# Performance work log

Measured on AMD Instinct MI355X. Metric: run time of the kernel, lower is better.

Reference implementation:

```python
import jax, jax.numpy as jnp
import numpy as np

EMBED = 1024
HEADS = 16
HDIM = 64
FFN = 4 * EMBED
EPS = 1e-5


def setup_inputs() -> dict:
    key = jax.random.key(0)
    ks = jax.random.split(key, 12)
    def lin(k, fan_in, shape):
        b = 1.0 / np.sqrt(fan_in)
        return jax.random.uniform(k, shape, jnp.float32, -b, b)
    return {
        "x": jax.random.normal(ks[0], (4, 2048, EMBED), jnp.float32),
        "Wq": lin(ks[1], EMBED, (EMBED, HEADS * HDIM)),
        "Wk": lin(ks[2], EMBED, (EMBED, HEADS * HDIM)),
        "Wv": lin(ks[3], EMBED, (EMBED, HEADS * HDIM)),
        "Wo": lin(ks[4], HEADS * HDIM, (HEADS * HDIM, EMBED)),
        "ln1_g": jnp.ones((EMBED,), jnp.float32),
        "ln1_b": jnp.zeros((EMBED,), jnp.float32),
        "ln2_g": jnp.ones((EMBED,), jnp.float32),
        "ln2_b": jnp.zeros((EMBED,), jnp.float32),
        "W1": lin(ks[5], EMBED, (EMBED, FFN)),
        "b1": lin(ks[6], EMBED, (FFN,)),
        "W2": lin(ks[7], FFN, (FFN, EMBED)),
        "b2": lin(ks[8], FFN, (EMBED,)),
    }


def _layer_norm(x, g, b):
    mu = jnp.mean(x, axis=-1, keepdims=True)
    var = jnp.var(x, axis=-1, keepdims=True)
    return (x - mu) * jax.lax.rsqrt(var + EPS) * g + b


def reference(x, Wq, Wk, Wv, Wo, ln1_g, ln1_b, ln2_g, ln2_b, W1, b1, W2, b2):
    B, S, _ = x.shape
    residual = x
    h = _layer_norm(x, ln1_g, ln1_b)
    # project and split heads: [B, H, S, Dh]
    q = (h @ Wq).reshape(B, S, HEADS, HDIM).transpose(0, 2, 1, 3)
    k = (h @ Wk).reshape(B, S, HEADS, HDIM).transpose(0, 2, 1, 3)
    v = (h @ Wv).reshape(B, S, HEADS, HDIM).transpose(0, 2, 1, 3)
    scale = HDIM ** -0.5
    scores = jnp.einsum("bhqd,bhkd->bhqk", q, k) * scale
    # causal mask (upper triangle excluded above diagonal -> -inf)
    mask = jnp.triu(jnp.ones((S, S), bool), k=1)
    scores = jnp.where(mask, -jnp.inf, scores)
    attn = jax.nn.softmax(scores, axis=-1)
    out = jnp.einsum("bhqk,bhkd->bhqd", attn, v)
    out = out.transpose(0, 2, 1, 3).reshape(B, S, HEADS * HDIM)
    x = residual + out @ Wo
    residual = x
    h = _layer_norm(x, ln2_g, ln2_b)
    h = jax.nn.gelu(h @ W1 + b1, approximate=False) @ W2 + b2
    return residual + h
```

## Files before the change

kernel.cpp:

```cpp
#include <hip/hip_runtime.h>
#include <hip/hip_bf16.h>
#include <math.h>

typedef __bf16 bf16;
typedef bf16 bf16x8 __attribute__((ext_vector_type(8)));
typedef bf16 bf16x4 __attribute__((ext_vector_type(4)));
typedef float f32x4 __attribute__((ext_vector_type(4)));

#define ROWS 8192
#define EMB  1024
#define NH   16
#define HD   64
#define FFN  4096
#define QKVN 3072
#define SEQ  2048

__device__ __forceinline__ void gl2lds16(const bf16* g, bf16* l) {
  __builtin_amdgcn_global_load_lds((const __attribute__((address_space(1))) void*)g,
                                   (__attribute__((address_space(3))) void*)l, 16, 0, 0);
}

__global__ void transpose_cast(const float* __restrict__ W, bf16* __restrict__ Wt,
                               int K, int N, float scale) {
  __shared__ float tile[32][33];
  const int n0 = blockIdx.x * 32, k0 = blockIdx.y * 32;
  const int tx = threadIdx.x & 31, ty = threadIdx.x >> 5;
#pragma unroll
  for (int i = 0; i < 32; i += 8)
    tile[ty + i][tx] = W[(size_t)(k0 + ty + i) * N + n0 + tx];
  __syncthreads();
#pragma unroll
  for (int i = 0; i < 32; i += 8)
    Wt[(size_t)(n0 + ty + i) * K + k0 + tx] = (bf16)(tile[tx][ty + i] * scale);
}

__global__ void v_transpose(const bf16* __restrict__ qkv, bf16* __restrict__ vt) {
  __shared__ bf16 tile[32][33];
  const int s0 = blockIdx.x * 32, d0 = blockIdx.y * 32, bh = blockIdx.z;
  const int b = bh >> 4, h = bh & 15;
  const int tx = threadIdx.x & 31, ty = threadIdx.x >> 5;
#pragma unroll
  for (int i = 0; i < 32; i += 8)
    tile[ty + i][tx] = qkv[(size_t)(b * SEQ + s0 + ty + i) * QKVN + 2 * EMB + h * HD + d0 + tx];
  __syncthreads();
#pragma unroll
  for (int i = 0; i < 32; i += 8)
    vt[(size_t)(bh * HD + d0 + ty + i) * SEQ + s0 + tx] = tile[tx][ty + i];
}

__global__ void layernorm_bf16(const float* __restrict__ x, const float* __restrict__ g,
                               const float* __restrict__ b, bf16* __restrict__ out) {
  const int row = blockIdx.x;
  const int t = threadIdx.x;
  const float4 v = ((const float4*)(x + (size_t)row * EMB))[t];
  float s = v.x + v.y + v.z + v.w;
  float ss = v.x * v.x + v.y * v.y + v.z * v.z + v.w * v.w;
#pragma unroll
  for (int off = 32; off; off >>= 1) {
    s += __shfl_down(s, off);
    ss += __shfl_down(ss, off);
  }
  __shared__ float sbuf[8];
  const int wave = t >> 6, lane = t & 63;
  if (lane == 0) { sbuf[wave] = s; sbuf[4 + wave] = ss; }
  __syncthreads();
  if (t == 0) {
    float S = sbuf[0] + sbuf[1] + sbuf[2] + sbuf[3];
    float SS = sbuf[4] + sbuf[5] + sbuf[6] + sbuf[7];
    float mu = S * (1.0f / EMB);
    float var = SS * (1.0f / EMB) - mu * mu;
    sbuf[0] = mu;
    sbuf[1] = rsqrtf(var + 1e-5f);
  }
  __syncthreads();
  const float mu = sbuf[0], rs = sbuf[1];
  const float4 gv = ((const float4*)g)[t];
  const float4 bv = ((const float4*)b)[t];
  bf16x4 o;
  o[0] = (bf16)((v.x - mu) * rs * gv.x + bv.x);
  o[1] = (bf16)((v.y - mu) * rs * gv.y + bv.y);
  o[2] = (bf16)((v.z - mu) * rs * gv.z + bv.z);
  o[3] = (bf16)((v.w - mu) * rs * gv.w + bv.w);
  *(bf16x4*)(out + (size_t)row * EMB + t * 4) = o;
}

template <int EPI, int N_, int K_>
__global__ __launch_bounds__(256, 2) void gemm_bt(
    const bf16* __restrict__ A, const bf16* __restrict__ Bt, void* __restrict__ C,
    const float* __restrict__ bias, const float* __restrict__ resid) {
  constexpr int N = N_, K = K_;
  __shared__ __align__(16) bf16 As[128 * 64];
  __shared__ __align__(16) bf16 Bs[128 * 64];
  const int tid = threadIdx.x;
  const int lane = tid & 63;
  const int wave = tid >> 6;
  const int wm = (wave >> 1) * 64;
  const int wn = (wave & 1) * 64;
  constexpr int tn = N / 128;
  const int lin = blockIdx.y * tn + blockIdx.x;
  const int grp = lin >> 3;
  const int m0 = ((grp / tn) * 8 + (lin & 7)) * 128;
  const int n0 = (grp % tn) * 128;
  const int quad = lane >> 4;
  const int l16 = lane & 15;
  const int srow8 = lane >> 3;
  const int scol = ((lane & 7) ^ srow8) * 8;
  const int xr = l16 & 7;

  const bf16* ap = A + (size_t)(m0 + wave * 32 + srow8) * K + scol;
  const bf16* bp = Bt + (size_t)(n0 + wave * 32 + srow8) * K + scol;
  bf16* const as0 = &As[wave * 32 * 64];
  bf16* const bs0 = &Bs[wave * 32 * 64];

  f32x4 acc[4][4] = {};

  for (int kt = 0; kt < K; kt += 64) {
    __syncthreads();
#pragma unroll
    for (int q = 0; q < 4; q++) {
      gl2lds16(ap + q * 8 * K, as0 + q * 8 * 64);
      gl2lds16(bp + q * 8 * K, bs0 + q * 8 * 64);
    }
    ap += 64;
    bp += 64;
    __syncthreads();
#pragma unroll
    for (int h = 0; h < 2; h++) {
      const int cp = ((h * 4 + quad) ^ xr) * 8;
      bf16x8 af[4], bfr[4];
#pragma unroll
      for (int i = 0; i < 4; i++)
        af[i] = *(const bf16x8*)&As[(wm + i * 16 + l16) * 64 + cp];
#pragma unroll
      for (int j = 0; j < 4; j++)
        bfr[j] = *(const bf16x8*)&Bs[(wn + j * 16 + l16) * 64 + cp];
#pragma unroll
      for (int i = 0; i < 4; i++)
#pragma unroll
        for (int j = 0; j < 4; j++)
          acc[i][j] = __builtin_amdgcn_mfma_f32_16x16x32_bf16(af[i], bfr[j], acc[i][j], 0, 0, 0);
    }
  }

#pragma unroll
  for (int i = 0; i < 4; i++)
#pragma unroll
    for (int j = 0; j < 4; j++)
#pragma unroll
      for (int r = 0; r < 4; r++) {
        const int row = m0 + wm + i * 16 + quad * 4 + r;
        const int col = n0 + wn + j * 16 + l16;
        const size_t idx = (size_t)row * N + col;
        float v = acc[i][j][r];
        if (EPI == 0) {
          ((bf16*)C)[idx] = (bf16)v;
        } else if (EPI == 1) {
          ((float*)C)[idx] = v + resid[idx];
        } else if (EPI == 2) {
          v += bias[col];
          const float u = 1.5957691216f * (v + 0.044715f * v * v * v);
          v = v / (1.0f + __expf(-u));
          ((bf16*)C)[idx] = (bf16)v;
        } else {
          ((float*)C)[idx] = v + bias[col] + resid[idx];
        }
      }
}

__global__ __launch_bounds__(256, 4) void flash_attn(
    const bf16* __restrict__ qkv, const bf16* __restrict__ vt, bf16* __restrict__ out) {
  const int pr = blockIdx.x;
  const int bh = blockIdx.y;
  const int b = bh >> 4, h = bh & 15;
  const int tid = threadIdx.x;
  const int lane = tid & 63, wave = tid >> 6;
  const int quad = lane >> 4, l16 = lane & 15;

  __shared__ __align__(16) bf16 Ks[64][72];
  __shared__ __align__(16) bf16 Vts[64][72];
  __shared__ __align__(16) bf16 Ps[4][16][72];

  const size_t rowbase = (size_t)b * SEQ;
  const int srow = tid >> 3;
  const int sc8 = (tid & 7) * 8;
  const bf16* kbase = qkv + rowbase * QKVN + EMB + h * HD;
  const bf16* vbase = vt + (size_t)(bh * HD) * SEQ;

#pragma unroll 1
  for (int half = 0; half < 2; half++) {
    const int qt = half ? pr : 31 - pr;
    const int qrow_a = qt * 64 + wave * 16 + l16;
    const bf16* qptr = qkv + (rowbase + qrow_a) * QKVN + h * HD;
    const bf16x8 qf0 = *(const bf16x8*)(qptr + quad * 8);
    const bf16x8 qf1 = *(const bf16x8*)(qptr + 32 + quad * 8);
    f32x4 o0 = {}, o1 = {}, o2 = {}, o3 = {};
    f32x4 lsum = {};
    const int qrow_c = qt * 64 + wave * 16 + quad * 4;

#pragma unroll 1
    for (int kt = 0; kt <= qt; kt++) {
      __syncthreads();
      *(bf16x8*)&Ks[srow][sc8] =
          *(const bf16x8*)(kbase + (size_t)(kt * 64 + srow) * QKVN + sc8);
      *(bf16x8*)&Ks[srow + 32][sc8] =
          *(const bf16x8*)(kbase + (size_t)(kt * 64 + srow + 32) * QKVN + sc8);
      *(bf16x8*)&Vts[srow][sc8] =
          *(const bf16x8*)(vbase + (size_t)srow * SEQ + kt * 64 + sc8);
      *(bf16x8*)&Vts[srow + 32][sc8] =
          *(const bf16x8*)(vbase + (size_t)(srow + 32) * SEQ + kt * 64 + sc8);
      __syncthreads();

      if (kt < qt) {
#pragma unroll
        for (int j = 0; j < 4; j++) {
          const bf16x8 kf0 = *(const bf16x8*)&Ks[j * 16 + l16][quad * 8];
          const bf16x8 kf1 = *(const bf16x8*)&Ks[j * 16 + l16][32 + quad * 8];
          f32x4 a = {};
          a = __builtin_amdgcn_mfma_f32_16x16x32_bf16(qf0, kf0, a, 0, 0, 0);
          a = __builtin_amdgcn_mfma_f32_16x16x32_bf16(qf1, kf1, a, 0, 0, 0);
#pragma unroll
          for (int r = 0; r < 4; r++) {
            const float pj = __expf(a[r]);
            lsum[r] += pj;
            Ps[wave][quad * 4 + r][j * 16 + l16] = (bf16)pj;
          }
        }
      } else {
#pragma unroll
        for (int j = 0; j < 4; j++) {
          if (j > wave) {
#pragma unroll
            for (int r = 0; r < 4; r++)
              Ps[wave][quad * 4 + r][j * 16 + l16] = (bf16)0.0f;
          } else {
            const bf16x8 kf0 = *(const bf16x8*)&Ks[j * 16 + l16][quad * 8];
            const bf16x8 kf1 = *(const bf16x8*)&Ks[j * 16 + l16][32 + quad * 8];
            f32x4 a = {};
            a = __builtin_amdgcn_mfma_f32_16x16x32_bf16(qf0, kf0, a, 0, 0, 0);
            a = __builtin_amdgcn_mfma_f32_16x16x32_bf16(qf1, kf1, a, 0, 0, 0);
            if (j == wave) {
#pragma unroll
              for (int r = 0; r < 4; r++) {
                const float v = (l16 > quad * 4 + r) ? -INFINITY : a[r];
                const float pj = __expf(v);
                lsum[r] += pj;
                Ps[wave][quad * 4 + r][j * 16 + l16] = (bf16)pj;
              }
            } else {
#pragma unroll
              for (int r = 0; r < 4; r++) {
                const float pj = __expf(a[r]);
                lsum[r] += pj;
                Ps[wave][quad * 4 + r][j * 16 + l16] = (bf16)pj;
              }
            }
          }
        }
      }

      const bf16x8 af0 = *(const bf16x8*)&Ps[wave][l16][quad * 8];
      const bf16x8 af1 = *(const bf16x8*)&Ps[wave][l16][32 + quad * 8];
      {
        const bf16x8 vf0 = *(const bf16x8*)&Vts[0 + l16][quad * 8];
        const bf16x8 vf1 = *(const bf16x8*)&Vts[0 + l16][32 + quad * 8];
        o0 = __builtin_amdgcn_mfma_f32_16x16x32_bf16(af0, vf0, o0, 0, 0, 0);
        o0 = __builtin_amdgcn_mfma_f32_16x16x32_bf16(af1, vf1, o0, 0, 0, 0);
      }
      {
        const bf16x8 vf0 = *(const bf16x8*)&Vts[16 + l16][quad * 8];
        const bf16x8 vf1 = *(const bf16x8*)&Vts[16 + l16][32 + quad * 8];
        o1 = __builtin_amdgcn_mfma_f32_16x16x32_bf16(af0, vf0, o1, 0, 0, 0);
        o1 = __builtin_amdgcn_mfma_f32_16x16x32_bf16(af1, vf1, o1, 0, 0, 0);
      }
      {
        const bf16x8 vf0 = *(const bf16x8*)&Vts[32 + l16][quad * 8];
        const bf16x8 vf1 = *(const bf16x8*)&Vts[32 + l16][32 + quad * 8];
        o2 = __builtin_amdgcn_mfma_f32_16x16x32_bf16(af0, vf0, o2, 0, 0, 0);
        o2 = __builtin_amdgcn_mfma_f32_16x16x32_bf16(af1, vf1, o2, 0, 0, 0);
      }
      {
        const bf16x8 vf0 = *(const bf16x8*)&Vts[48 + l16][quad * 8];
        const bf16x8 vf1 = *(const bf16x8*)&Vts[48 + l16][32 + quad * 8];
        o3 = __builtin_amdgcn_mfma_f32_16x16x32_bf16(af0, vf0, o3, 0, 0, 0);
        o3 = __builtin_amdgcn_mfma_f32_16x16x32_bf16(af1, vf1, o3, 0, 0, 0);
      }
    }

#pragma unroll
    for (int r = 0; r < 4; r++) {
      float ls = lsum[r];
      ls += __shfl_xor(ls, 1);
      ls += __shfl_xor(ls, 2);
      ls += __shfl_xor(ls, 4);
      ls += __shfl_xor(ls, 8);
      const float iv = 1.0f / ls;
      bf16* op = out + (rowbase + qrow_c + r) * EMB + h * HD;
      op[0 + l16] = (bf16)(o0[r] * iv);
      op[16 + l16] = (bf16)(o1[r] * iv);
      op[32 + l16] = (bf16)(o2[r] * iv);
      op[48 + l16] = (bf16)(o3[r] * iv);
    }
  }
}

extern "C" void kernel_launch(void* const* d_in, const int* in_sizes, int n_in,
                              void* d_out, int out_size, void* d_ws, size_t ws_size,
                              hipStream_t stream) {
  const float* x     = (const float*)d_in[0];
  const float* Wq    = (const float*)d_in[1];
  const float* Wk    = (const float*)d_in[2];
  const float* Wv    = (const float*)d_in[3];
  const float* Wo    = (const float*)d_in[4];
  const float* ln1_g = (const float*)d_in[5];
  const float* ln1_b = (const float*)d_in[6];
  const float* ln2_g = (const float*)d_in[7];
  const float* ln2_b = (const float*)d_in[8];
  const float* W1    = (const float*)d_in[9];
  const float* b1    = (const float*)d_in[10];
  const float* W2    = (const float*)d_in[11];
  const float* b2    = (const float*)d_in[12];
  float* out = (float*)d_out;

  bf16* p = (bf16*)d_ws;
  bf16* wqkv_t = p;                 p += (size_t)QKVN * EMB;
  bf16* wo_t   = p;                 p += (size_t)EMB * EMB;
  bf16* w1_t   = p;                 p += (size_t)FFN * EMB;
  bf16* w2_t   = p;                 p += (size_t)EMB * FFN;
  bf16* h      = p;                 p += (size_t)ROWS * EMB;
  bf16* qkv    = p;                 p += (size_t)ROWS * QKVN;
  bf16* attn_o = p;                 p += (size_t)ROWS * EMB;
  bf16* ffn1   = p;
  bf16* vt     = h;

  transpose_cast<<<dim3(32, 32), 256, 0, stream>>>(Wq, wqkv_t, EMB, EMB, 0.125f);
  transpose_cast<<<dim3(32, 32), 256, 0, stream>>>(Wk, wqkv_t + (size_t)EMB * EMB, EMB, EMB, 1.0f);
  transpose_cast<<<dim3(32, 32), 256, 0, stream>>>(Wv, wqkv_t + (size_t)2 * EMB * EMB, EMB, EMB, 1.0f);
  transpose_cast<<<dim3(32, 32), 256, 0, stream>>>(Wo, wo_t, EMB, EMB, 1.0f);
  transpose_cast<<<dim3(128, 32), 256, 0, stream>>>(W1, w1_t, EMB, FFN, 1.0f);
  transpose_cast<<<dim3(32, 128), 256, 0, stream>>>(W2, w2_t, FFN, EMB, 1.0f);

  layernorm_bf16<<<ROWS, 256, 0, stream>>>(x, ln1_g, ln1_b, h);

  gemm_bt<0, QKVN, EMB><<<dim3(QKVN / 128, ROWS / 128), 256, 0, stream>>>(
      h, wqkv_t, qkv, nullptr, nullptr);

  v_transpose<<<dim3(SEQ / 32, HD / 32, 64), 256, 0, stream>>>(qkv, vt);

  flash_attn<<<dim3(16, 64), 256, 0, stream>>>(qkv, vt, attn_o);

  gemm_bt<1, EMB, EMB><<<dim3(EMB / 128, ROWS / 128), 256, 0, stream>>>(
      attn_o, wo_t, out, nullptr, x);

  layernorm_bf16<<<ROWS, 256, 0, stream>>>(out, ln2_g, ln2_b, h);

  gemm_bt<2, FFN, EMB><<<dim3(FFN / 128, ROWS / 128), 256, 0, stream>>>(
      h, w1_t, ffn1, b1, nullptr);

  gemm_bt<3, EMB, FFN><<<dim3(EMB / 128, ROWS / 128), 256, 0, stream>>>(
      ffn1, w2_t, out, b2, out);
}
```

Before: 489.3 us.

## Map GEMM and attention blocks to XCDs, use direct LDS loads in attention

Block indices in the GEMM and the attention kernel are remapped so that blocks landing on the same XCD (lin & 7) share M-rows or heads, which should improve L2 reuse on the chiplet layout. The attention kernel now loads its K and V tiles with global_load_lds into an XOR-swizzled unpadded LDS layout instead of register round-trips into padded arrays. The launch-bounds occupancy hint is raised from 4 to 6 and the grid is flattened to 1D. The new mapping assumes the grid sizes divide cleanly into 8-way XCD groups, and the swizzled reads must match the load pattern exactly.

```diff
diff --git a/kernel.cpp b/kernel.cpp
--- a/kernel.cpp
+++ b/kernel.cpp
@@ -98,9 +98,10 @@
   const int wn = (wave & 1) * 64;
   constexpr int tn = N / 128;
   const int lin = blockIdx.y * tn + blockIdx.x;
-  const int grp = lin >> 3;
-  const int m0 = ((grp / tn) * 8 + (lin & 7)) * 128;
-  const int n0 = (grp % tn) * 128;
+  const int xcd = lin & 7;
+  const int idx = lin >> 3;
+  const int m0 = (xcd * 8 + (idx & 7)) * 128;
+  const int n0 = (idx >> 3) * 128;
   const int quad = lane >> 4;
   const int l16 = lane & 15;
   const int srow8 = lane >> 3;
@@ -150,39 +151,43 @@
       for (int r = 0; r < 4; r++) {
         const int row = m0 + wm + i * 16 + quad * 4 + r;
         const int col = n0 + wn + j * 16 + l16;
-        const size_t idx = (size_t)row * N + col;
+        const size_t idx2 = (size_t)row * N + col;
         float v = acc[i][j][r];
         if (EPI == 0) {
-          ((bf16*)C)[idx] = (bf16)v;
+          ((bf16*)C)[idx2] = (bf16)v;
         } else if (EPI == 1) {
-          ((float*)C)[idx] = v + resid[idx];
+          ((float*)C)[idx2] = v + resid[idx2];
         } else if (EPI == 2) {
           v += bias[col];
           const float u = 1.5957691216f * (v + 0.044715f * v * v * v);
           v = v / (1.0f + __expf(-u));
-          ((bf16*)C)[idx] = (bf16)v;
+          ((bf16*)C)[idx2] = (bf16)v;
         } else {
-          ((float*)C)[idx] = v + bias[col] + resid[idx];
+          ((float*)C)[idx2] = v + bias[col] + resid[idx2];
         }
       }
 }
 
-__global__ __launch_bounds__(256, 4) void flash_attn(
+__global__ __launch_bounds__(256, 6) void flash_attn(
     const bf16* __restrict__ qkv, const bf16* __restrict__ vt, bf16* __restrict__ out) {
-  const int pr = blockIdx.x;
-  const int bh = blockIdx.y;
+  const int bid = blockIdx.x;
+  const int xcd = bid & 7;
+  const int idx = bid >> 3;
+  const int pr = idx & 15;
+  const int bh = xcd + ((idx >> 4) << 3);
   const int b = bh >> 4, h = bh & 15;
   const int tid = threadIdx.x;
   const int lane = tid & 63, wave = tid >> 6;
   const int quad = lane >> 4, l16 = lane & 15;
 
-  __shared__ __align__(16) bf16 Ks[64][72];
-  __shared__ __align__(16) bf16 Vts[64][72];
+  __shared__ __align__(16) bf16 Ks[64 * 64];
+  __shared__ __align__(16) bf16 Vts[64 * 64];
   __shared__ __align__(16) bf16 Ps[4][16][72];
 
   const size_t rowbase = (size_t)b * SEQ;
-  const int srow = tid >> 3;
-  const int sc8 = (tid & 7) * 8;
+  const int s8 = (lane >> 3) & 7;
+  const int cs = ((lane & 7) ^ s8) * 8;
+  const int xk = l16 & 7;
   const bf16* kbase = qkv + rowbase * QKVN + EMB + h * HD;
   const bf16* vbase = vt + (size_t)(bh * HD) * SEQ;
 
@@ -197,24 +202,24 @@
     f32x4 lsum = {};
     const int qrow_c = qt * 64 + wave * 16 + quad * 4;
 
+    const bf16* kp = kbase + (size_t)(wave * 8 + s8) * QKVN + cs;
+    const bf16* vp = vbase + (size_t)(wave * 8 + s8) * SEQ + cs;
+
 #pragma unroll 1
     for (int kt = 0; kt <= qt; kt++) {
       __syncthreads();
-      *(bf16x8*)&Ks[srow][sc8] =
-          *(const bf16x8*)(kbase + (size_t)(kt * 64 + srow) * QKVN + sc8);
-      *(bf16x8*)&Ks[srow + 32][sc8] =
-          *(const bf16x8*)(kbase + (size_t)(kt * 64 + srow + 32) * QKVN + sc8);
-      *(bf16x8*)&Vts[srow][sc8] =
-          *(const bf16x8*)(vbase + (size_t)srow * SEQ + kt * 64 + sc8);
-      *(bf16x8*)&Vts[srow + 32][sc8] =
-          *(const bf16x8*)(vbase + (size_t)(srow + 32) * SEQ + kt * 64 + sc8);
+      gl2lds16(kp + (size_t)kt * 64 * QKVN, &Ks[(wave * 8) * 64]);
+      gl2lds16(kp + (size_t)(kt * 64 + 32) * QKVN, &Ks[(32 + wave * 8) * 64]);
+      gl2lds16(vp + kt * 64, &Vts[(wave * 8) * 64]);
+      gl2lds16(vp + (size_t)32 * SEQ + kt * 64, &Vts[(32 + wave * 8) * 64]);
       __syncthreads();
 
       if (kt < qt) {
 #pragma unroll
         for (int j = 0; j < 4; j++) {
-          const bf16x8 kf0 = *(const bf16x8*)&Ks[j * 16 + l16][quad * 8];
-          const bf16x8 kf1 = *(const bf16x8*)&Ks[j * 16 + l16][32 + quad * 8];
+          const int rr = (j * 16 + l16) * 64;
+          const bf16x8 kf0 = *(const bf16x8*)&Ks[rr + (quad ^ xk) * 8];
+          const bf16x8 kf1 = *(const bf16x8*)&Ks[rr + ((4 + quad) ^ xk) * 8];
           f32x4 a = {};
           a = __builtin_amdgcn_mfma_f32_16x16x32_bf16(qf0, kf0, a, 0, 0, 0);
           a = __builtin_amdgcn_mfma_f32_16x16x32_bf16(qf1, kf1, a, 0, 0, 0);
@@ -233,8 +238,9 @@
             for (int r = 0; r < 4; r++)
               Ps[wave][quad * 4 + r][j * 16 + l16] = (bf16)0.0f;
           } else {
-            const bf16x8 kf0 = *(const bf16x8*)&Ks[j * 16 + l16][quad * 8];
-            const bf16x8 kf1 = *(const bf16x8*)&Ks[j * 16 + l16][32 + quad * 8];
+            const int rr = (j * 16 + l16) * 64;
+            const bf16x8 kf0 = *(const bf16x8*)&Ks[rr + (quad ^ xk) * 8];
+            const bf16x8 kf1 = *(const bf16x8*)&Ks[rr + ((4 + quad) ^ xk) * 8];
             f32x4 a = {};
             a = __builtin_amdgcn_mfma_f32_16x16x32_bf16(qf0, kf0, a, 0, 0, 0);
             a = __builtin_amdgcn_mfma_f32_16x16x32_bf16(qf1, kf1, a, 0, 0, 0);
@@ -260,29 +266,14 @@
 
       const bf16x8 af0 = *(const bf16x8*)&Ps[wave][l16][quad * 8];
       const bf16x8 af1 = *(const bf16x8*)&Ps[wave][l16][32 + quad * 8];
-      {
-        const bf16x8 vf0 = *(const bf16x8*)&Vts[0 + l16][quad * 8];
-        const bf16x8 vf1 = *(const bf16x8*)&Vts[0 + l16][32 + quad * 8];
-        o0 = __builtin_amdgcn_mfma_f32_16x16x32_bf16(af0, vf0, o0, 0, 0, 0);
-        o0 = __builtin_amdgcn_mfma_f32_16x16x32_bf16(af1, vf1, o0, 0, 0, 0);
-      }
-      {
-        const bf16x8 vf0 = *(const bf16x8*)&Vts[16 + l16][quad * 8];
-        const bf16x8 vf1 = *(const bf16x8*)&Vts[16 + l16][32 + quad * 8];
-        o1 = __builtin_amdgcn_mfma_f32_16x16x32_bf16(af0, vf0, o1, 0, 0, 0);
-        o1 = __builtin_amdgcn_mfma_f32_16x16x32_bf16(af1, vf1, o1, 0, 0, 0);
-      }
-      {
-        const bf16x8 vf0 = *(const bf16x8*)&Vts[32 + l16][quad * 8];
-        const bf16x8 vf1 = *(const bf16x8*)&Vts[32 + l16][32 + quad * 8];
-        o2 = __builtin_amdgcn_mfma_f32_16x16x32_bf16(af0, vf0, o2, 0, 0, 0);
-        o2 = __builtin_amdgcn_mfma_f32_16x16x32_bf16(af1, vf1, o2, 0, 0, 0);
-      }
-      {
-        const bf16x8 vf0 = *(const bf16x8*)&Vts[48 + l16][quad * 8];
-        const bf16x8 vf1 = *(const bf16x8*)&Vts[48 + l16][32 + quad * 8];
-        o3 = __builtin_amdgcn_mfma_f32_16x16x32_bf16(af0, vf0, o3, 0, 0, 0);
-        o3 = __builtin_amdgcn_mfma_f32_16x16x32_bf16(af1, vf1, o3, 0, 0, 0);
+#pragma unroll
+      for (int j = 0; j < 4; j++) {
+        const int rr = (j * 16 + l16) * 64;
+        const bf16x8 vf0 = *(const bf16x8*)&Vts[rr + (quad ^ xk) * 8];
+        const bf16x8 vf1 = *(const bf16x8*)&Vts[rr + ((4 + quad) ^ xk) * 8];
+        f32x4& oj = (j == 0) ? o0 : (j == 1) ? o1 : (j == 2) ? o2 : o3;
+        oj = __builtin_amdgcn_mfma_f32_16x16x32_bf16(af0, vf0, oj, 0, 0, 0);
+        oj = __builtin_amdgcn_mfma_f32_16x16x32_bf16(af1, vf1, oj, 0, 0, 0);
       }
     }
 
@@ -346,7 +337,7 @@
 
   v_transpose<<<dim3(SEQ / 32, HD / 32, 64), 256, 0, stream>>>(qkv, vt);
 
-  flash_attn<<<dim3(16, 64), 256, 0, stream>>>(qkv, vt, attn_o);
+  flash_attn<<<1024, 256, 0, stream>>>(qkv, vt, attn_o);
 
   gemm_bt<1, EMB, EMB><<<dim3(EMB / 128, ROWS / 128), 256, 0, stream>>>(
       attn_o, wo_t, out, nullptr, x);
```

After: 448.3 us. 8.4% less time.
